# Kernel tuning notes

Hardware: AMD Instinct MI355X
Metric: run time of the kernel (lower is better)

Reference implementation:

```python
import jax, jax.numpy as jnp
import numpy as np

N = 8192
IN_C = 512
OUT_C = 512


def setup_inputs() -> dict:
    key = jax.random.key(0)
    k1, k2, k3 = jax.random.split(key, 3)
    x = jax.random.normal(k1, (N, IN_C), dtype=jnp.float32)
    adj = jax.random.uniform(k2, (N, N), dtype=jnp.float32)
    # torch.rand initializer for the weight (uniform [0,1))
    w = jax.random.uniform(k3, (IN_C, OUT_C), dtype=jnp.float32)
    return {"x": x, "adj": adj, "w": w}


def reference(x, adj, w):
    # A = adj + I
    A = adj + jnp.eye(adj.shape[0], dtype=adj.dtype)
    # D_hat = diag(deg)^{-1/2}; diagonal inverse + sqrt == elementwise rsqrt of degrees
    deg = jnp.sum(A, axis=1)                      # [N]
    d_inv_sqrt = jax.lax.rsqrt(deg)               # [N]
    # A_hat = D_hat @ A @ D_hat == row/col scaling (same math, no dense inverse)
    A_hat = A * d_inv_sqrt[:, None] * d_inv_sqrt[None, :]
    mm_1 = A_hat @ x                              # [N, in_c]
    return jax.nn.elu(mm_1 @ w)                   # [N, out_c]
```

## Files before the change

kernel.cpp:

```cpp
#include <hip/hip_runtime.h>

#define NN 8192
#define CC 512

typedef __attribute__((ext_vector_type(8))) short short8;
typedef __attribute__((ext_vector_type(4))) float f32x4;
typedef unsigned short ushort_t;

__device__ __forceinline__ unsigned short f2bf(float f) {
    unsigned int u = __float_as_uint(f);
    u += 0x7FFF + ((u >> 16) & 1);
    return (unsigned short)(u >> 16);
}
__device__ __forceinline__ float bf2f(unsigned short u) {
    return __uint_as_float(((unsigned int)u) << 16);
}

__device__ __forceinline__ void gload_lds16(const void* g, void* l) {
    __builtin_amdgcn_global_load_lds((const __attribute__((address_space(1))) unsigned int*)g,
                                     (__attribute__((address_space(3))) unsigned int*)l,
                                     16, 0, 0);
}

__global__ __launch_bounds__(256) void k_pre(const float* __restrict__ x,
                                             const float* __restrict__ adj,
                                             const ushort_t* __restrict__ wt,
                                             float* __restrict__ ds,
                                             ushort_t* __restrict__ adj16,
                                             float* __restrict__ z) {
    __shared__ __align__(16) ushort_t As[128 * 64];
    __shared__ __align__(16) ushort_t Bs[128 * 64];
    __shared__ float partial[4];

    int t = threadIdx.x;
    if (blockIdx.x >= 256) {
        int row = blockIdx.x - 256;
        const float4* p = (const float4*)(adj + (size_t)row * NN);
        ushort4* q = (ushort4*)(adj16 + (size_t)row * NN);
        float s = 0.f;
#pragma unroll
        for (int i = 0; i < 8; ++i) {
            float4 v = p[t + i * 256];
            s += (v.x + v.y) + (v.z + v.w);
            ushort4 u;
            u.x = f2bf(v.x); u.y = f2bf(v.y); u.z = f2bf(v.z); u.w = f2bf(v.w);
            q[t + i * 256] = u;
        }
#pragma unroll
        for (int off = 32; off > 0; off >>= 1) s += __shfl_down(s, off, 64);
        if ((t & 63) == 0) partial[t >> 6] = s;
        __syncthreads();
        if (t == 0) {
            float deg = ((partial[0] + partial[1]) + (partial[2] + partial[3])) + 1.0f;
            ds[row] = rsqrtf(deg);
        }
        return;
    }

    int bid = blockIdx.x;
    int wid = t >> 6, lane = t & 63;
    int cb = bid & 3, rb = bid >> 2;
    int rowBase = rb * 128, colBase = cb * 128;

    int ar = t >> 4, ac4 = t & 15;
    const float* aptr = x + (size_t)(rowBase + ar) * CC + ac4 * 4;
    int srow0 = t >> 3, ss = t & 7;

    f32x4 acc[4][4] = {};
    int wr = wid >> 1, wc = wid & 1;
    int fr = lane & 15, fq = lane >> 4;

    for (int kt = 0; kt < CC / 64; ++kt) {
#pragma unroll
        for (int i2 = 0; i2 < 8; ++i2) {
            float4 v = *(const float4*)(aptr + kt * 64 + (size_t)i2 * 16 * CC);
            int row = i2 * 16 + ar;
            ushort4 u2;
            u2.x = f2bf(v.x); u2.y = f2bf(v.y); u2.z = f2bf(v.z); u2.w = f2bf(v.w);
            *(ushort4*)((char*)As + row * 128 + ((ac4 * 8) ^ ((row & 7) << 4))) = u2;
        }
#pragma unroll
        for (int j = 0; j < 4; ++j) {
            int row = j * 32 + srow0;
            gload_lds16((const char*)(wt + (size_t)(colBase + row) * CC + kt * 64 +
                                      ((ss ^ (row & 7)) << 3)),
                        (char*)Bs + j * 4096 + wid * 1024);
        }
        __syncthreads();
#pragma unroll
        for (int ks = 0; ks < 2; ++ks) {
            short8 af[4], bfv[4];
#pragma unroll
            for (int m = 0; m < 4; ++m) {
                int row = wr * 64 + m * 16 + fr;
                af[m] = *(const short8*)((const char*)As + row * 128 +
                                         ((ks * 64 + fq * 16) ^ ((row & 7) << 4)));
            }
#pragma unroll
            for (int n = 0; n < 4; ++n) {
                int col = wc * 64 + n * 16 + fr;
                bfv[n] = *(const short8*)((const char*)Bs + col * 128 +
                                          ((ks * 64 + fq * 16) ^ ((col & 7) << 4)));
            }
#pragma unroll
            for (int m = 0; m < 4; ++m)
#pragma unroll
                for (int n = 0; n < 4; ++n)
                    acc[m][n] = __builtin_amdgcn_mfma_f32_16x16x32_bf16(af[m], bfv[n], acc[m][n], 0, 0, 0);
        }
        __syncthreads();
    }

#pragma unroll
    for (int m = 0; m < 4; ++m) {
#pragma unroll
        for (int j = 0; j < 4; ++j) {
            int gr = rowBase + wr * 64 + m * 16 + fq * 4 + j;
#pragma unroll
            for (int n = 0; n < 4; ++n) {
                int gc = colBase + wc * 64 + n * 16 + fr;
                z[(size_t)gr * CC + gc] = acc[m][n][j];
            }
        }
    }
}

__global__ __launch_bounds__(256) void k_rowsum(const float* __restrict__ adj,
                                                float* __restrict__ ds) {
    int row = blockIdx.x;
    const float4* p = (const float4*)(adj + (size_t)row * NN);
    float s = 0.f;
#pragma unroll
    for (int i = 0; i < 8; ++i) {
        float4 v = p[threadIdx.x + i * 256];
        s += (v.x + v.y) + (v.z + v.w);
    }
#pragma unroll
    for (int off = 32; off > 0; off >>= 1) s += __shfl_down(s, off, 64);
    __shared__ float partial[4];
    if ((threadIdx.x & 63) == 0) partial[threadIdx.x >> 6] = s;
    __syncthreads();
    if (threadIdx.x == 0) {
        float deg = ((partial[0] + partial[1]) + (partial[2] + partial[3])) + 1.0f;
        ds[row] = rsqrtf(deg);
    }
}

__global__ __launch_bounds__(256) void k_transpose(const float* __restrict__ in,
                                                   ushort_t* __restrict__ out,
                                                   const float* __restrict__ scale,
                                                   int R, int C) {
    __shared__ float tile[64][65];
    int r0 = blockIdx.x * 64, c0 = blockIdx.y * 64;
    int t = threadIdx.x;
    int cl = t & 63;
    int rl0 = t >> 6;
#pragma unroll
    for (int i = 0; i < 16; ++i) {
        int r = rl0 + i * 4;
        float v = in[(size_t)(r0 + r) * C + c0 + cl];
        float sc = scale ? scale[r0 + r] : 1.0f;
        tile[r][cl] = v * sc;
    }
    __syncthreads();
#pragma unroll
    for (int i = 0; i < 16; ++i) {
        int c = rl0 + i * 4;
        int r = cl;
        out[(size_t)(c0 + c) * R + r0 + r] = f2bf(tile[r][c]);
    }
}

template <bool ELU>
__global__ __launch_bounds__(256, 2) void k_gemm2t(const ushort_t* __restrict__ A,
                                                   const ushort_t* __restrict__ Bt,
                                                   float* __restrict__ out) {
    __shared__ __align__(16) ushort_t As[128 * 64];
    __shared__ __align__(16) ushort_t Bs[128 * 64];

    int t = threadIdx.x;
    int wid = t >> 6, lane = t & 63;
    int bid = blockIdx.x;
    bid = (bid & 7) * 32 + (bid >> 3);
    int cb = bid & 3, rb = bid >> 2;
    int rowBase = rb * 128, colBase = cb * 128;

    int srow0 = t >> 3, ss = t & 7;

    f32x4 acc[4][4] = {};
    int wr = wid >> 1, wc = wid & 1;
    int fr = lane & 15, fq = lane >> 4;

    for (int kt = 0; kt < CC / 64; ++kt) {
#pragma unroll
        for (int j = 0; j < 4; ++j) {
            int row = j * 32 + srow0;
            gload_lds16((const char*)(A + (size_t)(rowBase + row) * CC + kt * 64 +
                                      ((ss ^ (row & 7)) << 3)),
                        (char*)As + j * 4096 + wid * 1024);
            gload_lds16((const char*)(Bt + (size_t)(colBase + row) * CC + kt * 64 +
                                      ((ss ^ (row & 7)) << 3)),
                        (char*)Bs + j * 4096 + wid * 1024);
        }
        __syncthreads();
#pragma unroll
        for (int ks = 0; ks < 2; ++ks) {
            short8 af[4], bfv[4];
#pragma unroll
            for (int m = 0; m < 4; ++m) {
                int row = wr * 64 + m * 16 + fr;
                af[m] = *(const short8*)((const char*)As + row * 128 +
                                         ((ks * 64 + fq * 16) ^ ((row & 7) << 4)));
            }
#pragma unroll
            for (int n = 0; n < 4; ++n) {
                int col = wc * 64 + n * 16 + fr;
                bfv[n] = *(const short8*)((const char*)Bs + col * 128 +
                                          ((ks * 64 + fq * 16) ^ ((col & 7) << 4)));
            }
#pragma unroll
            for (int m = 0; m < 4; ++m)
#pragma unroll
                for (int n = 0; n < 4; ++n)
                    acc[m][n] = __builtin_amdgcn_mfma_f32_16x16x32_bf16(af[m], bfv[n], acc[m][n], 0, 0, 0);
        }
        __syncthreads();
    }

#pragma unroll
    for (int m = 0; m < 4; ++m) {
#pragma unroll
        for (int j = 0; j < 4; ++j) {
            int gr = rowBase + wr * 64 + m * 16 + fq * 4 + j;
#pragma unroll
            for (int n = 0; n < 4; ++n) {
                int gc = colBase + wc * 64 + n * 16 + fr;
                float v = acc[m][n][j];
                out[(size_t)gr * CC + gc] = ELU ? (v > 0.f ? v : expm1f(v)) : v;
            }
        }
    }
}

__global__ __launch_bounds__(512, 4) void k_gemm1e(const ushort_t* __restrict__ adj16,
                                                   const ushort_t* __restrict__ yt2,
                                                   ushort_t* __restrict__ part16) {
    __shared__ __align__(16) ushort_t Al[3][256 * 32];
    __shared__ __align__(16) ushort_t Bl[3][128 * 32];

    int t = threadIdx.x;
    int wid = t >> 6, lane = t & 63;
    int fr = lane & 15, fq = lane >> 4;

    int gid = blockIdx.x;
    int xcd = gid & 7, slot = gid >> 3;
    int cb = slot & 3;
    int v = (slot >> 2) + 16 * xcd;
    int rb = v & 31, ks = v >> 5;
    int rowBase = rb * 256, colBase = cb * 128;
    int kt0 = ks * 64;

    int wr = wid >> 1, wc = wid & 1;
    int srow = t >> 2;
    int sw = ((t & 3) ^ ((srow >> 1) & 3)) << 3;
    const ushort_t* aBase = adj16 + (size_t)(rowBase + srow) * NN + sw;
    const ushort_t* bBase = yt2 + (size_t)(colBase + srow) * NN + sw;

    auto stage = [&](int buf, int tile) {
        gload_lds16(aBase + (size_t)tile * 32, (char*)Al[buf] + wid * 1024);
        gload_lds16(aBase + (size_t)128 * NN + (size_t)tile * 32, (char*)Al[buf] + 8192 + wid * 1024);
        gload_lds16(bBase + (size_t)tile * 32, (char*)Bl[buf] + wid * 1024);
    };

    f32x4 acc[4][4] = {};
    int sws = (fq ^ ((fr >> 1) & 3)) << 4;

    stage(0, kt0 + 0);
    stage(1, kt0 + 1);
    asm volatile("s_waitcnt vmcnt(3)" ::: "memory");
    __builtin_amdgcn_sched_barrier(0);
    __builtin_amdgcn_s_barrier();

    int cur = 0, nxt = 2;
    for (int i = 0; i < 64; ++i) {
        const char* Ab = (const char*)Al[cur] + wr * 4096;
        const char* Bb = (const char*)Bl[cur] + wc * 4096;

        short8 af[4], bfv[4];
#pragma unroll
        for (int m = 0; m < 4; ++m)
            af[m] = *(const short8*)(Ab + (m * 16 + fr) * 64 + sws);
#pragma unroll
        for (int n = 0; n < 4; ++n)
            bfv[n] = *(const short8*)(Bb + (n * 16 + fr) * 64 + sws);

        stage(nxt, kt0 + ((i + 2) & 63));

        __builtin_amdgcn_s_setprio(1);
#pragma unroll
        for (int m = 0; m < 4; ++m)
#pragma unroll
            for (int n = 0; n < 4; ++n)
                acc[m][n] = __builtin_amdgcn_mfma_f32_16x16x32_bf16(af[m], bfv[n], acc[m][n], 0, 0, 0);
        __builtin_amdgcn_s_setprio(0);

        asm volatile("s_waitcnt vmcnt(3)" ::: "memory");
        __builtin_amdgcn_sched_barrier(0);
        __builtin_amdgcn_s_barrier();

        cur = cur == 2 ? 0 : cur + 1;
        nxt = nxt == 2 ? 0 : nxt + 1;
    }

#pragma unroll
    for (int m = 0; m < 4; ++m) {
#pragma unroll
        for (int jj = 0; jj < 4; ++jj) {
            int gr = rowBase + wr * 64 + m * 16 + fq * 4 + jj;
            ushort_t* dst = part16 + ((size_t)ks * NN + gr) * CC + colBase;
#pragma unroll
            for (int n = 0; n < 4; ++n)
                dst[wc * 64 + n * 16 + fr] = f2bf(acc[m][n][jj]);
        }
    }
}

__global__ __launch_bounds__(256) void k_finish2(const ushort_t* __restrict__ part16,
                                                 const float* __restrict__ ds,
                                                 const float* __restrict__ z,
                                                 float* __restrict__ out) {
    size_t i = (size_t)blockIdx.x * 256 + threadIdx.x;
    const size_t stride = (size_t)NN * CC / 4;
    float s0 = 0.f, s1 = 0.f, s2 = 0.f, s3 = 0.f;
#pragma unroll
    for (int k = 0; k < 4; ++k) {
        ushort4 p = ((const ushort4*)part16)[i + k * stride];
        s0 += bf2f(p.x); s1 += bf2f(p.y); s2 += bf2f(p.z); s3 += bf2f(p.w);
    }
    int row = (int)(i >> 7);
    float d = ds[row];
    float d2 = d * d;
    f32x4 zv = ((const f32x4*)z)[i];
    f32x4 o;
    float v;
    v = d * s0 + d2 * zv[0]; o[0] = v > 0.f ? v : expm1f(v);
    v = d * s1 + d2 * zv[1]; o[1] = v > 0.f ? v : expm1f(v);
    v = d * s2 + d2 * zv[2]; o[2] = v > 0.f ? v : expm1f(v);
    v = d * s3 + d2 * zv[3]; o[3] = v > 0.f ? v : expm1f(v);
    ((f32x4*)out)[i] = o;
}

__global__ __launch_bounds__(256, 4) void k_gemm1_fb(const float* __restrict__ adj,
                                                     const ushort_t* __restrict__ yt,
                                                     const float* __restrict__ ds,
                                                     const float* __restrict__ x,
                                                     ushort_t* __restrict__ mm1) {
    __shared__ __align__(16) ushort_t As[128 * 64];
    __shared__ __align__(16) ushort_t Bs[128 * 64];

    int t = threadIdx.x;
    int wid = t >> 6, lane = t & 63;
    int bid = blockIdx.x;
    bid = (bid & 7) * 32 + (bid >> 3);
    int colBase = (bid & 3) * 128;
    int rowBase = (bid >> 2) * 128;

    int ar = t >> 4;
    int ac4 = t & 15;
    const float* aptr = adj + (size_t)(rowBase + ar) * NN + ac4 * 4;
    int brow0 = t >> 3;
    int bs = t & 7;
    float4 areg[8];

    auto loadA = [&](int kt) {
        const float* p = aptr + kt * 64;
#pragma unroll
        for (int i = 0; i < 8; ++i)
            areg[i] = *(const float4*)(p + (size_t)i * 16 * NN);
    };
    auto writeA = [&]() {
#pragma unroll
        for (int i = 0; i < 8; ++i) {
            int row = i * 16 + ar;
            ushort4 u;
            u.x = f2bf(areg[i].x); u.y = f2bf(areg[i].y);
            u.z = f2bf(areg[i].z); u.w = f2bf(areg[i].w);
            *(ushort4*)((char*)As + row * 128 + ((ac4 * 8) ^ ((row & 7) << 4))) = u;
        }
    };

    f32x4 acc[4][4] = {};
    int wr = wid >> 1, wc = wid & 1;
    int fr = lane & 15, fq = lane >> 4;

    loadA(0);
    for (int kt = 0; kt < NN / 64; ++kt) {
        writeA();
#pragma unroll
        for (int j = 0; j < 4; ++j) {
            int row = j * 32 + brow0;
            gload_lds16((const char*)(yt + (size_t)(colBase + row) * NN + kt * 64 +
                                      ((bs ^ (row & 7)) << 3)),
                        (char*)Bs + j * 4096 + wid * 1024);
        }
        __syncthreads();
        if (kt + 1 < NN / 64) loadA(kt + 1);
#pragma unroll
        for (int ks2 = 0; ks2 < 2; ++ks2) {
            short8 af[4], bfv[4];
#pragma unroll
            for (int m = 0; m < 4; ++m) {
                int row = wr * 64 + m * 16 + fr;
                af[m] = *(const short8*)((const char*)As + row * 128 +
                                         ((ks2 * 64 + fq * 16) ^ ((row & 7) << 4)));
            }
#pragma unroll
            for (int n = 0; n < 4; ++n) {
                int col = wc * 64 + n * 16 + fr;
                bfv[n] = *(const short8*)((const char*)Bs + col * 128 +
                                          ((ks2 * 64 + fq * 16) ^ ((col & 7) << 4)));
            }
#pragma unroll
            for (int m = 0; m < 4; ++m)
#pragma unroll
                for (int n = 0; n < 4; ++n)
                    acc[m][n] = __builtin_amdgcn_mfma_f32_16x16x32_bf16(af[m], bfv[n], acc[m][n], 0, 0, 0);
        }
        __syncthreads();
    }

#pragma unroll
    for (int m = 0; m < 4; ++m) {
#pragma unroll
        for (int j = 0; j < 4; ++j) {
            int gr = rowBase + wr * 64 + m * 16 + fq * 4 + j;
            float dsr = ds[gr];
#pragma unroll
            for (int n = 0; n < 4; ++n) {
                int gc = colBase + wc * 64 + n * 16 + fr;
                float v = dsr * (acc[m][n][j] + dsr * x[(size_t)gr * CC + gc]);
                mm1[(size_t)gr * CC + gc] = f2bf(v);
            }
        }
    }
}

extern "C" void kernel_launch(void* const* d_in, const int* in_sizes, int n_in,
                              void* d_out, int out_size, void* d_ws, size_t ws_size,
                              hipStream_t stream) {
    const float* x   = (const float*)d_in[0];
    const float* adj = (const float*)d_in[1];
    const float* w   = (const float*)d_in[2];
    float* out = (float*)d_out;

    char* ws = (char*)d_ws;
    size_t off = 0;
    float*    ds  = (float*)(ws + off);  off += 32u << 10;
    ushort_t* yt  = (ushort_t*)(ws + off);  off += 8u << 20;
    ushort_t* wt  = (ushort_t*)(ws + off);  off += 512u << 10;
    ushort_t* xb  = (ushort_t*)(ws + off);  off += 8u << 20;
    float*    z   = (float*)(ws + off);  off += 16u << 20;
    ushort_t* part16 = (ushort_t*)(ws + off);  off += 32u << 20;
    ushort_t* adj16  = (ushort_t*)(ws + off);
    const size_t adjBytes = (size_t)NN * NN * 2;

    if (ws_size >= off + adjBytes) {
        k_transpose<<<dim3(CC / 64, CC / 64), 256, 0, stream>>>(w, wt, nullptr, CC, CC);
        k_pre<<<NN + 256, 256, 0, stream>>>(x, adj, wt, ds, adj16, z);
        k_transpose<<<dim3(NN / 64, CC / 64), 256, 0, stream>>>(z, yt, ds, NN, CC);
        k_gemm1e<<<512, 512, 0, stream>>>(adj16, yt, part16);
        k_finish2<<<NN * CC / 4 / 256, 256, 0, stream>>>(part16, ds, z, out);
    } else {
        ushort_t* mm1 = xb;
        k_rowsum<<<NN, 256, 0, stream>>>(adj, ds);
        k_transpose<<<dim3(NN / 64, CC / 64), 256, 0, stream>>>(x, yt, ds, NN, CC);
        k_transpose<<<dim3(CC / 64, CC / 64), 256, 0, stream>>>(w, wt, nullptr, CC, CC);
        k_gemm1_fb<<<256, 256, 0, stream>>>(adj, yt, ds, x, mm1);
        k_gemm2t<true><<<256, 256, 0, stream>>>(mm1, wt, out);
    }
}
```

Measured before the change: 195.7 us.

## Fuse adj fp32-to-bf16 conversion into GEMM A-tile loading, drop adj16 buffer

The pre-pass no longer writes a bf16 copy of the 8192x8192 adjacency matrix. The main GEMM instead loads fp32 adj tiles into registers, converts them with packed bf16 instructions, and writes them to LDS. This removes a 128 MB write and re-read of adj16. In exchange the GEMM reads twice the bytes per A tile, since it reads fp32, and each A tile is read by the four column-block workgroups. The A buffer also drops from triple to double buffering with register staging, which may expose more load latency.

```diff
diff --git a/kernel.cpp b/kernel.cpp
--- a/kernel.cpp
+++ b/kernel.cpp
@@ -5,6 +5,7 @@
 
 typedef __attribute__((ext_vector_type(8))) short short8;
 typedef __attribute__((ext_vector_type(4))) float f32x4;
+typedef __attribute__((ext_vector_type(4))) unsigned int u32x4;
 typedef unsigned short ushort_t;
 
 __device__ __forceinline__ unsigned short f2bf(float f) {
@@ -15,6 +16,11 @@
 __device__ __forceinline__ float bf2f(unsigned short u) {
     return __uint_as_float(((unsigned int)u) << 16);
 }
+__device__ __forceinline__ unsigned int cvt_pk_bf16(float lo, float hi) {
+    unsigned int r;
+    asm("v_cvt_pk_bf16_f32 %0, %1, %2" : "=v"(r) : "v"(lo), "v"(hi));
+    return r;
+}
 
 __device__ __forceinline__ void gload_lds16(const void* g, void* l) {
     __builtin_amdgcn_global_load_lds((const __attribute__((address_space(1))) unsigned int*)g,
@@ -26,7 +32,6 @@
                                              const float* __restrict__ adj,
                                              const ushort_t* __restrict__ wt,
                                              float* __restrict__ ds,
-                                             ushort_t* __restrict__ adj16,
                                              float* __restrict__ z) {
     __shared__ __align__(16) ushort_t As[128 * 64];
     __shared__ __align__(16) ushort_t Bs[128 * 64];
@@ -36,15 +41,11 @@
     if (blockIdx.x >= 256) {
         int row = blockIdx.x - 256;
         const float4* p = (const float4*)(adj + (size_t)row * NN);
-        ushort4* q = (ushort4*)(adj16 + (size_t)row * NN);
         float s = 0.f;
 #pragma unroll
         for (int i = 0; i < 8; ++i) {
             float4 v = p[t + i * 256];
             s += (v.x + v.y) + (v.z + v.w);
-            ushort4 u;
-            u.x = f2bf(v.x); u.y = f2bf(v.y); u.z = f2bf(v.z); u.w = f2bf(v.w);
-            q[t + i * 256] = u;
         }
 #pragma unroll
         for (int off = 32; off > 0; off >>= 1) s += __shfl_down(s, off, 64);
@@ -242,10 +243,10 @@
     }
 }
 
-__global__ __launch_bounds__(512, 4) void k_gemm1e(const ushort_t* __restrict__ adj16,
+__global__ __launch_bounds__(512, 4) void k_gemm1f(const float* __restrict__ adj,
                                                    const ushort_t* __restrict__ yt2,
                                                    ushort_t* __restrict__ part16) {
-    __shared__ __align__(16) ushort_t Al[3][256 * 32];
+    __shared__ __align__(16) ushort_t Al[2][256 * 32];
     __shared__ __align__(16) ushort_t Bl[3][128 * 32];
 
     int t = threadIdx.x;
@@ -261,31 +262,56 @@
     int kt0 = ks * 64;
 
     int wr = wid >> 1, wc = wid & 1;
+
+    int arow = t >> 1, ah = t & 1;
+    const float* aSrc = adj + (size_t)(rowBase + arow) * NN + ah * 16;
+    int aswz = (arow >> 1) & 3;
+    int ac0 = ((ah * 2 + 0) ^ aswz) * 16;
+    int ac1 = ((ah * 2 + 1) ^ aswz) * 16;
+
     int srow = t >> 2;
     int sw = ((t & 3) ^ ((srow >> 1) & 3)) << 3;
-    const ushort_t* aBase = adj16 + (size_t)(rowBase + srow) * NN + sw;
     const ushort_t* bBase = yt2 + (size_t)(colBase + srow) * NN + sw;
 
-    auto stage = [&](int buf, int tile) {
-        gload_lds16(aBase + (size_t)tile * 32, (char*)Al[buf] + wid * 1024);
-        gload_lds16(aBase + (size_t)128 * NN + (size_t)tile * 32, (char*)Al[buf] + 8192 + wid * 1024);
+    float4 ra0, ra1, ra2, ra3;
+    auto loadA = [&](int tile) {
+        const float4* p = (const float4*)(aSrc + (size_t)tile * 32);
+        ra0 = p[0]; ra1 = p[1]; ra2 = p[2]; ra3 = p[3];
+    };
+    auto writeA = [&](int buf) {
+        u32x4 c0, c1;
+        c0[0] = cvt_pk_bf16(ra0.x, ra0.y); c0[1] = cvt_pk_bf16(ra0.z, ra0.w);
+        c0[2] = cvt_pk_bf16(ra1.x, ra1.y); c0[3] = cvt_pk_bf16(ra1.z, ra1.w);
+        c1[0] = cvt_pk_bf16(ra2.x, ra2.y); c1[1] = cvt_pk_bf16(ra2.z, ra2.w);
+        c1[2] = cvt_pk_bf16(ra3.x, ra3.y); c1[3] = cvt_pk_bf16(ra3.z, ra3.w);
+        char* base = (char*)Al[buf] + arow * 64;
+        *(u32x4*)(base + ac0) = c0;
+        *(u32x4*)(base + ac1) = c1;
+    };
+    auto stageB = [&](int buf, int tile) {
         gload_lds16(bBase + (size_t)tile * 32, (char*)Bl[buf] + wid * 1024);
     };
 
     f32x4 acc[4][4] = {};
     int sws = (fq ^ ((fr >> 1) & 3)) << 4;
 
-    stage(0, kt0 + 0);
-    stage(1, kt0 + 1);
-    asm volatile("s_waitcnt vmcnt(3)" ::: "memory");
+    loadA(kt0 + 0);
+    stageB(0, kt0 + 0);
+    asm volatile("s_waitcnt vmcnt(1)" ::: "memory");
+    __builtin_amdgcn_sched_barrier(0);
+    writeA(0);
+    stageB(1, kt0 + 1);
+    loadA(kt0 + 1);
+    asm volatile("s_waitcnt vmcnt(5)" ::: "memory");
+    asm volatile("s_waitcnt lgkmcnt(0)" ::: "memory");
     __builtin_amdgcn_sched_barrier(0);
     __builtin_amdgcn_s_barrier();
 
-    int cur = 0, nxt = 2;
     for (int i = 0; i < 64; ++i) {
-        const char* Ab = (const char*)Al[cur] + wr * 4096;
-        const char* Bb = (const char*)Bl[cur] + wc * 4096;
-
+        stageB((i + 2) % 3, kt0 + ((i + 2) & 63));
+
+        const char* Ab = (const char*)Al[i & 1] + wr * 4096;
+        const char* Bb = (const char*)Bl[i % 3] + wc * 4096;
         short8 af[4], bfv[4];
 #pragma unroll
         for (int m = 0; m < 4; ++m)
@@ -293,8 +319,6 @@
 #pragma unroll
         for (int n = 0; n < 4; ++n)
             bfv[n] = *(const short8*)(Bb + (n * 16 + fr) * 64 + sws);
-
-        stage(nxt, kt0 + ((i + 2) & 63));
 
         __builtin_amdgcn_s_setprio(1);
 #pragma unroll
@@ -304,12 +328,13 @@
                 acc[m][n] = __builtin_amdgcn_mfma_f32_16x16x32_bf16(af[m], bfv[n], acc[m][n], 0, 0, 0);
         __builtin_amdgcn_s_setprio(0);
 
-        asm volatile("s_waitcnt vmcnt(3)" ::: "memory");
+        asm volatile("s_waitcnt vmcnt(1)" ::: "memory");
+        __builtin_amdgcn_sched_barrier(0);
+        writeA((i + 1) & 1);
+        loadA(kt0 + ((i + 2) & 63));
+        asm volatile("s_waitcnt lgkmcnt(0)" ::: "memory");
         __builtin_amdgcn_sched_barrier(0);
         __builtin_amdgcn_s_barrier();
-
-        cur = cur == 2 ? 0 : cur + 1;
-        nxt = nxt == 2 ? 0 : nxt + 1;
     }
 
 #pragma unroll
@@ -461,14 +486,12 @@
     ushort_t* xb  = (ushort_t*)(ws + off);  off += 8u << 20;
     float*    z   = (float*)(ws + off);  off += 16u << 20;
     ushort_t* part16 = (ushort_t*)(ws + off);  off += 32u << 20;
-    ushort_t* adj16  = (ushort_t*)(ws + off);
-    const size_t adjBytes = (size_t)NN * NN * 2;
-
-    if (ws_size >= off + adjBytes) {
+
+    if (ws_size >= off) {
         k_transpose<<<dim3(CC / 64, CC / 64), 256, 0, stream>>>(w, wt, nullptr, CC, CC);
-        k_pre<<<NN + 256, 256, 0, stream>>>(x, adj, wt, ds, adj16, z);
+        k_pre<<<NN + 256, 256, 0, stream>>>(x, adj, wt, ds, z);
         k_transpose<<<dim3(NN / 64, CC / 64), 256, 0, stream>>>(z, yt, ds, NN, CC);
-        k_gemm1e<<<512, 512, 0, stream>>>(adj16, yt, part16);
+        k_gemm1f<<<512, 512, 0, stream>>>(adj, yt, part16);
         k_finish2<<<NN * CC / 4 / 256, 256, 0, stream>>>(part16, ds, z, out);
     } else {
         ushort_t* mm1 = xb;
```

After: 218.5 us. 11.6% more time.
